# Kernel tuning notes

Measured on AMD Instinct MI355X. Metric: run time of the kernel, lower is better.

## Reference

```python
import jax, jax.numpy as jnp
import numpy as np

IMG = 512      # diffusion image side
CUT_SIZE = 224 # CLIP input resolution
CUTN = 64
CUT_POW = 1.0


def setup_inputs() -> dict:
    key = jax.random.key(0)
    k1, k2, k3, k4 = jax.random.split(key, 4)
    B, C, H, W = 4, 3, IMG, IMG
    x = jax.random.normal(k1, (B, C, H, W), dtype=jnp.float32)
    max_size = min(H, W)
    min_size = min(H, W, CUT_SIZE)
    # size = int(rand()**cut_pow * (max_size - min_size) + min_size)
    u = jax.random.uniform(k2, (CUTN,))
    sizes = ((u ** CUT_POW) * (max_size - min_size) + min_size).astype(jnp.int32)
    # offsets uniform in [0, side - size]
    offsetx = (jax.random.uniform(k3, (CUTN,)) * (W - sizes + 1).astype(jnp.float32)).astype(jnp.int32)
    offsety = (jax.random.uniform(k4, (CUTN,)) * (H - sizes + 1).astype(jnp.float32)).astype(jnp.int32)
    return {"x": x, "sizes": sizes, "offsetx": offsetx, "offsety": offsety, "cut_size": CUT_SIZE}


def _make_cutouts(x, sizes, offsetx, offsety, S):
    # Fused batched crop + bilinear resize (torch F.interpolate, align_corners=False).
    B, C, H, W = x.shape
    N = sizes.shape[0]
    sizes_f = sizes.astype(x.dtype)
    # source coords within the crop: (j + 0.5) * size/S - 0.5, clamped at 0
    grid = jnp.arange(S, dtype=x.dtype) + 0.5                      # [S]
    src = jnp.maximum(sizes_f[:, None] / S * grid[None, :] - 0.5, 0.0)  # [N,S]
    i0 = jnp.floor(src).astype(jnp.int32)
    frac = src - i0.astype(x.dtype)                                # [N,S]
    i0 = jnp.minimum(i0, sizes[:, None] - 1)
    i1 = jnp.minimum(i0 + 1, sizes[:, None] - 1)
    # global indices into the full image (crops are square: same grid for y and x)
    Y0 = (offsety[:, None] + i0)[:, :, None]  # [N,S,1]
    Y1 = (offsety[:, None] + i1)[:, :, None]
    X0 = (offsetx[:, None] + i0)[:, None, :]  # [N,1,S]
    X1 = (offsetx[:, None] + i1)[:, None, :]
    wy = frac[:, :, None]                      # [N,S,1]
    wx = frac[:, None, :]                      # [N,1,S]
    # four-corner gather: each is [B,C,N,S,S]
    v00 = x[:, :, Y0, X0]
    v01 = x[:, :, Y0, X1]
    v10 = x[:, :, Y1, X0]
    v11 = x[:, :, Y1, X1]
    out = (v00 * (1 - wy) * (1 - wx) + v01 * (1 - wy) * wx
           + v10 * wy * (1 - wx) + v11 * wy * wx)
    # torch.cat over cutouts -> cutout-major: [N*B, C, S, S]
    return out.transpose(2, 0, 1, 3, 4).reshape(N * B, C, S, S)


def reference(x, sizes, offsetx, offsety, cut_size):
    return _make_cutouts(x, sizes, offsetx, offsety, cut_size)
```

## Files before the change

kernel.cpp:

```cpp
#include <hip/hip_runtime.h>

constexpr int S  = 224;
constexpr int B  = 4;
constexpr int C  = 3;
constexpr int H  = 512;
constexpr int W  = 512;
constexpr int N  = 64;
constexpr int PLANES = B * C;
constexpr int HROWS  = S / 2;
constexpr int PAIRS_PER_HP  = N * (HROWS / 2);
constexpr int PAIRS_PER_XCD = 3 * PAIRS_PER_HP;
constexpr int WPB    = 4;
constexpr int BLOCKS_PER_XCD = PAIRS_PER_XCD / WPB;
constexpr int GRID   = 8 * BLOCKS_PER_XCD;

__device__ __forceinline__ void load_lds16(const float* g, float* l) {
    __builtin_amdgcn_global_load_lds(
        (const __attribute__((address_space(1))) void*)g,
        (__attribute__((address_space(3))) void*)l,
        16, 0, 0);
}

__device__ __forceinline__ void stage_row(const float* plane, int oy, int i,
                                          float scale, int sz, int lane,
                                          float* buf, float& fy_out) {
    const float sy  = fmaxf(scale * ((float)i + 0.5f) - 0.5f, 0.0f);
    const float fiy = floorf(sy);
    fy_out = sy - fiy;
    const int iy0 = min((int)fiy, sz - 1);
    const int iy1 = min(iy0 + 1, sz - 1);
    const float* r0 = plane + (size_t)(oy + iy0) * W;
    const float* r1 = plane + (size_t)(oy + iy1) * W;
    load_lds16(r0 + lane * 4,       buf);
    load_lds16(r0 + 256 + lane * 4, buf + 256);
    load_lds16(r1 + lane * 4,       buf + W);
    load_lds16(r1 + 256 + lane * 4, buf + W + 256);
}

__device__ __forceinline__ void compute_row(const float* buf, float fy, float scale,
                                            int sz, int ox, int lane, float* orow) {
    const float* l0 = buf;
    const float* l1 = buf + W;
    #pragma unroll
    for (int r = 0; r < 4; ++r) {
        const int px = r * 64 + lane;
        if (r < 3 || px < S) {
            const float sx  = fmaxf(scale * ((float)px + 0.5f) - 0.5f, 0.0f);
            const float fix = floorf(sx);
            const float fx  = sx - fix;
            const int   ix  = min((int)fix, sz - 1) + ox;
            const float v00 = l0[ix], v01 = l0[ix + 1];
            const float v10 = l1[ix], v11 = l1[ix + 1];
            const float top = v00 + (v01 - v00) * fx;
            const float bot = v10 + (v11 - v10) * fx;
            orow[px] = top + (bot - top) * fy;
        }
    }
}

__global__ __launch_bounds__(256) void cutouts_kernel(
    const float* __restrict__ x,
    const int*   __restrict__ sizes,
    const int*   __restrict__ offx,
    const int*   __restrict__ offy,
    float*       __restrict__ out)
{
    __shared__ float lds[WPB][2][2 * W];

    const int lane = threadIdx.x & 63;
    const int wv   = threadIdx.x >> 6;

    const int k     = blockIdx.x & 7;
    const int pair  = (blockIdx.x >> 3) * WPB + wv;
    const int hpsel = pair / PAIRS_PER_HP;
    const int rem   = pair - hpsel * PAIRS_PER_HP;
    const int n     = rem / (HROWS / 2);
    const int mp    = rem - n * (HROWS / 2);
    const int hp    = k + (hpsel << 3);
    const int pi    = hp >> 1;
    const int i0    = (hp & 1) * HROWS + 2 * mp;
    const int i1    = i0 + 1;

    const int   sz    = sizes[n];
    const float scale = (float)sz * (1.0f / (float)S);
    const int   oy    = offy[n];
    const int   ox    = offx[n];
    const float* plane = x + (size_t)pi * (H * W);

    float fy0, fy1;
    stage_row(plane, oy, i0, scale, sz, lane, &lds[wv][0][0], fy0);
    stage_row(plane, oy, i1, scale, sz, lane, &lds[wv][1][0], fy1);

    float* obase = out + (size_t)(n * PLANES + pi) * (S * S);

    asm volatile("s_waitcnt vmcnt(4)" ::: "memory");
    __builtin_amdgcn_sched_barrier(0);
    compute_row(&lds[wv][0][0], fy0, scale, sz, ox, lane, obase + (size_t)i0 * S);

    asm volatile("s_waitcnt vmcnt(4)" ::: "memory");
    __builtin_amdgcn_sched_barrier(0);
    compute_row(&lds[wv][1][0], fy1, scale, sz, ox, lane, obase + (size_t)i1 * S);
}

extern "C" void kernel_launch(void* const* d_in, const int* in_sizes, int n_in,
                              void* d_out, int out_size, void* d_ws, size_t ws_size,
                              hipStream_t stream) {
    const float* x     = (const float*)d_in[0];
    const int*   sizes = (const int*)d_in[1];
    const int*   offx  = (const int*)d_in[2];
    const int*   offy  = (const int*)d_in[3];
    float* out = (float*)d_out;

    cutouts_kernel<<<GRID, 256, 0, stream>>>(x, sizes, offx, offy, out);
}
```

Baseline: 45.26 us.

## Separate vertical and horizontal interpolation passes with crop-limited vector loads

Each wave now loads only the 16-byte chunks that cover the crop's columns, using registers rather than direct global-to-LDS copies. It blends the two source rows vertically in registers, writes one blended row to LDS, and runs a horizontal pass that emits float4 stores. This cuts global read traffic for small crops and halves LDS reads per output, at the cost of losing the async LDS load overlap and adding branching on crop width. Edge handling now clamps the row index to sz-2 and shifts the fraction to compensate.

```diff
diff --git a/kernel.cpp b/kernel.cpp
--- a/kernel.cpp
+++ b/kernel.cpp
@@ -1,60 +1,44 @@
 #include <hip/hip_runtime.h>
+#include <stdint.h>
 
-constexpr int S  = 224;
-constexpr int B  = 4;
-constexpr int C  = 3;
-constexpr int H  = 512;
-constexpr int W  = 512;
-constexpr int N  = 64;
-constexpr int PLANES = B * C;
-constexpr int HROWS  = S / 2;
+constexpr int S   = 224;
+constexpr int Wim = 512;
+constexpr int PLANES = 12;
+constexpr int N   = 64;
+constexpr int HROWS = S / 2;
 constexpr int PAIRS_PER_HP  = N * (HROWS / 2);
 constexpr int PAIRS_PER_XCD = 3 * PAIRS_PER_HP;
-constexpr int WPB    = 4;
+constexpr int WPB   = 4;
 constexpr int BLOCKS_PER_XCD = PAIRS_PER_XCD / WPB;
-constexpr int GRID   = 8 * BLOCKS_PER_XCD;
+constexpr int GRID  = 8 * BLOCKS_PER_XCD;
+constexpr int BUFD  = 544;
 
-__device__ __forceinline__ void load_lds16(const float* g, float* l) {
-    __builtin_amdgcn_global_load_lds(
-        (const __attribute__((address_space(1))) void*)g,
-        (__attribute__((address_space(3))) void*)l,
-        16, 0, 0);
+typedef float f32x4 __attribute__((ext_vector_type(4)));
+
+__device__ __forceinline__ void vparams(int i, float scale, int sz,
+                                        int& ay, float& fy) {
+    const float sy  = fmaxf(scale * ((float)i + 0.5f) - 0.5f, 0.0f);
+    const float fiy = floorf(sy);
+    const int   iy0 = (int)fiy;
+    ay = min(iy0, sz - 2);
+    fy = (sy - fiy) + (float)(iy0 - ay);
 }
 
-__device__ __forceinline__ void stage_row(const float* plane, int oy, int i,
-                                          float scale, int sz, int lane,
-                                          float* buf, float& fy_out) {
-    const float sy  = fmaxf(scale * ((float)i + 0.5f) - 0.5f, 0.0f);
-    const float fiy = floorf(sy);
-    fy_out = sy - fiy;
-    const int iy0 = min((int)fiy, sz - 1);
-    const int iy1 = min(iy0 + 1, sz - 1);
-    const float* r0 = plane + (size_t)(oy + iy0) * W;
-    const float* r1 = plane + (size_t)(oy + iy1) * W;
-    load_lds16(r0 + lane * 4,       buf);
-    load_lds16(r0 + 256 + lane * 4, buf + 256);
-    load_lds16(r1 + lane * 4,       buf + W);
-    load_lds16(r1 + 256 + lane * 4, buf + W + 256);
-}
-
-__device__ __forceinline__ void compute_row(const float* buf, float fy, float scale,
-                                            int sz, int ox, int lane, float* orow) {
-    const float* l0 = buf;
-    const float* l1 = buf + W;
-    #pragma unroll
-    for (int r = 0; r < 4; ++r) {
-        const int px = r * 64 + lane;
-        if (r < 3 || px < S) {
-            const float sx  = fmaxf(scale * ((float)px + 0.5f) - 0.5f, 0.0f);
+__device__ __forceinline__ void hpass(const float* buf, int shift, float scale,
+                                      int lane, float* orow) {
+    if (lane < 56) {
+        const int pxb = 4 * lane;
+        f32x4 o;
+        #pragma unroll
+        for (int r = 0; r < 4; ++r) {
+            const float sx  = fmaxf(scale * ((float)(pxb + r) + 0.5f) - 0.5f, 0.0f);
             const float fix = floorf(sx);
             const float fx  = sx - fix;
-            const int   ix  = min((int)fix, sz - 1) + ox;
-            const float v00 = l0[ix], v01 = l0[ix + 1];
-            const float v10 = l1[ix], v11 = l1[ix + 1];
-            const float top = v00 + (v01 - v00) * fx;
-            const float bot = v10 + (v11 - v10) * fx;
-            orow[px] = top + (bot - top) * fy;
+            const int   d   = shift + (int)fix;
+            const float v0 = buf[d], v1 = buf[d + 1];
+            o[r] = v0 + (v1 - v0) * fx;
         }
+        *(f32x4*)(orow + pxb) = o;
     }
 }
 
@@ -65,7 +49,7 @@
     const int*   __restrict__ offy,
     float*       __restrict__ out)
 {
-    __shared__ float lds[WPB][2][2 * W];
+    __shared__ float lds[WPB][2][BUFD];
 
     const int lane = threadIdx.x & 63;
     const int wv   = threadIdx.x >> 6;
@@ -79,27 +63,68 @@
     const int hp    = k + (hpsel << 3);
     const int pi    = hp >> 1;
     const int i0    = (hp & 1) * HROWS + 2 * mp;
-    const int i1    = i0 + 1;
 
     const int   sz    = sizes[n];
-    const float scale = (float)sz * (1.0f / (float)S);
+    const float scale = (float)sz / (float)S;
     const int   oy    = offy[n];
     const int   ox    = offx[n];
-    const float* plane = x + (size_t)pi * (H * W);
+    const float* plane = x + (size_t)pi * (Wim * Wim);
 
-    float fy0, fy1;
-    stage_row(plane, oy, i0, scale, sz, lane, &lds[wv][0][0], fy0);
-    stage_row(plane, oy, i1, scale, sz, lane, &lds[wv][1][0], fy1);
+    const int base4  = ox >> 2;
+    const int shift  = ox & 3;
+    const int lastc4 = 127 - base4;
+    const int K4     = (shift + sz + 5) >> 2;
+    const bool hi    = K4 > 64;
 
+    int ay0, ay1; float fy0, fy1;
+    vparams(i0,     scale, sz, ay0, fy0);
+    vparams(i0 + 1, scale, sz, ay1, fy1);
+
+    const int cA = min(lane, lastc4);
+    const int cB = min(lane + 64, lastc4);
+
+    const float* rA = plane + (size_t)(oy + ay0) * Wim + 4 * base4;
+    const float* rB = plane + (size_t)(oy + ay1) * Wim + 4 * base4;
+
+    f32x4 p00 = *(const f32x4*)(rA + 4 * cA);
+    f32x4 p01 = *(const f32x4*)(rA + Wim + 4 * cA);
+    f32x4 p10 = *(const f32x4*)(rB + 4 * cA);
+    f32x4 p11 = *(const f32x4*)(rB + Wim + 4 * cA);
+    f32x4 q00{}, q01{}, q10{}, q11{};
+    if (hi) {
+        q00 = *(const f32x4*)(rA + 4 * cB);
+        q01 = *(const f32x4*)(rA + Wim + 4 * cB);
+        q10 = *(const f32x4*)(rB + 4 * cB);
+        q11 = *(const f32x4*)(rB + Wim + 4 * cB);
+    }
+
+    float* buf0 = &lds[wv][0][0];
+    float* buf1 = &lds[wv][1][0];
     float* obase = out + (size_t)(n * PLANES + pi) * (S * S);
 
-    asm volatile("s_waitcnt vmcnt(4)" ::: "memory");
-    __builtin_amdgcn_sched_barrier(0);
-    compute_row(&lds[wv][0][0], fy0, scale, sz, ox, lane, obase + (size_t)i0 * S);
+    {
+        f32x4 w = p00 + (p01 - p00) * fy0;
+        if (lane > lastc4) w = f32x4{0.f, 0.f, 0.f, 0.f};
+        *(f32x4*)(buf0 + 4 * lane) = w;
+        if (hi) {
+            f32x4 wh = q00 + (q01 - q00) * fy0;
+            if (lane + 64 > lastc4) wh = f32x4{0.f, 0.f, 0.f, 0.f};
+            *(f32x4*)(buf0 + 4 * (lane + 64)) = wh;
+        }
+    }
+    hpass(buf0, shift, scale, lane, obase + (size_t)i0 * S);
 
-    asm volatile("s_waitcnt vmcnt(4)" ::: "memory");
-    __builtin_amdgcn_sched_barrier(0);
-    compute_row(&lds[wv][1][0], fy1, scale, sz, ox, lane, obase + (size_t)i1 * S);
+    {
+        f32x4 w = p10 + (p11 - p10) * fy1;
+        if (lane > lastc4) w = f32x4{0.f, 0.f, 0.f, 0.f};
+        *(f32x4*)(buf1 + 4 * lane) = w;
+        if (hi) {
+            f32x4 wh = q10 + (q11 - q10) * fy1;
+            if (lane + 64 > lastc4) wh = f32x4{0.f, 0.f, 0.f, 0.f};
+            *(f32x4*)(buf1 + 4 * (lane + 64)) = wh;
+        }
+    }
+    hpass(buf1, shift, scale, lane, obase + (size_t)(i0 + 1) * S);
 }
 
 extern "C" void kernel_launch(void* const* d_in, const int* in_sizes, int n_in,
```

Result: faster. 43.26 us (-4.4%).
